# Performance work log

Measured on AMD Instinct MI355X. Metric: run time of the kernel, lower is better.

The kernel has to match this reference:

```python
import jax, jax.numpy as jnp
import numpy as np
from jax import lax

EPS = 1e-5

# Straight-through identity binarization (torch code mutates .data, so autograd
# sees binarized values but grads flow as identity to the latent weights/inputs).
def ste_sign(x):
    return x + lax.stop_gradient(jnp.sign(x) - x)

# SignActivation: sign forward, hard-tanh-style gradient (zero where |i| > 1).
@jax.custom_vjp
def sign_act(x):
    return jnp.sign(x)

def _sa_fwd(x):
    return jnp.sign(x), x

def _sa_bwd(x, g):
    return (jnp.where(jnp.abs(x) <= 1.0, g, 0.0),)

sign_act.defvjp(_sa_fwd, _sa_bwd)

def bn2d(x, gamma, beta):
    # training-mode BatchNorm2d: batch stats over (N,H,W), biased variance
    mean = jnp.mean(x, axis=(0, 2, 3), keepdims=True)
    var = jnp.var(x, axis=(0, 2, 3), keepdims=True)
    xn = (x - mean) * lax.rsqrt(var + EPS)
    return xn * gamma.reshape(1, -1, 1, 1) + beta.reshape(1, -1, 1, 1)

def bn1d(x, gamma, beta):
    mean = jnp.mean(x, axis=0, keepdims=True)
    var = jnp.var(x, axis=0, keepdims=True)
    xn = (x - mean) * lax.rsqrt(var + EPS)
    return xn * gamma[None, :] + beta[None, :]

def conv2d(x, w, stride, pad):
    return lax.conv_general_dilated(
        x, w, window_strides=(stride, stride),
        padding=((pad, pad), (pad, pad)),
        dimension_numbers=("NCHW", "OIHW", "NCHW"))


def setup_inputs() -> dict:
    key = jax.random.key(0)
    ks = jax.random.split(key, 4)
    width = 0.01
    x = jax.random.normal(ks[0], (8192, 1, 28, 28), dtype=jnp.float32)
    w1 = jax.random.normal(ks[1], (32, 1, 5, 5), dtype=jnp.float32) * width
    w2 = jax.random.normal(ks[2], (64, 32, 4, 4), dtype=jnp.float32) * width
    w3 = jax.random.normal(ks[3], (10, 64 * 64), dtype=jnp.float32) * width
    g1 = jnp.ones((32,), jnp.float32); b1 = jnp.zeros((32,), jnp.float32)
    g2 = jnp.ones((64,), jnp.float32); b2 = jnp.zeros((64,), jnp.float32)
    g3 = jnp.ones((10,), jnp.float32); b3 = jnp.zeros((10,), jnp.float32)
    return {"x": x, "w1": w1, "g1": g1, "b1": b1,
            "w2": w2, "g2": g2, "b2": b2,
            "w3": w3, "g3": g3, "b3": b3}


def reference(x, w1, g1, b1, w2, g2, b2, w3, g3, b3):
    # cv1: input channels = 1 != 3 -> input binarized; weight binarized
    h = conv2d(ste_sign(x), ste_sign(w1), stride=2, pad=2)   # [B,32,14,14]
    h = bn2d(h, g1, b1)
    h = sign_act(h)
    # cv2: input channels 32 != 3 -> binarized (no-op on +-1 values)
    h = conv2d(ste_sign(h), ste_sign(w2), stride=2, pad=2)   # [B,64,8,8]
    h = bn2d(h, g2, b2)
    h = sign_act(h)
    h = h.reshape(h.shape[0], -1)                            # [B,4096]
    # fc3: features 4096 != 784 -> binarized (no-op on +-1 values)
    h = jnp.dot(ste_sign(h), ste_sign(w3).T)                 # [B,10]
    h = bn1d(h, g3, b3)
    return h
```

## Files before the change

kernel.cpp:

```cpp
#include <hip/hip_runtime.h>
#include <stdint.h>


#define NB 8192
typedef unsigned long long ull;

#define OFF_C1  ((size_t)0)
#define SZ_C1   ((size_t)NB*6272)
#define OFF_C2  (OFF_C1 + SZ_C1)
#define SZ_C2   ((size_t)NB*4096)
#define OFF_FC  (OFF_C2 + SZ_C2)
#define SZ_FC   ((size_t)NB*10*4)
#define OFF_S1  (OFF_FC + SZ_FC)
#define OFF_S2  (OFF_S1 + 2048)
#define OFF_S3  (OFF_S2 + 8192)
#define OFF_W2B (OFF_S3 + 2048)
#define OFF_W3B (OFF_W2B + 4096)

__device__ inline void mk_thresh(double s, double t, int &T, int &flip) {
    if (s > 0.0) {
        int v = (int)floor(-t / s) - 2;
        for (int c = 0; c < 6; ++c) { if (s * (double)v + t > 0.0) break; ++v; }
        T = v; flip = 0;
    } else if (s < 0.0) {
        int v = (int)floor(-t / s) - 2;
        for (int c = 0; c < 6; ++c) { if (!(s * (double)v + t > 0.0)) break; ++v; }
        T = v; flip = 1;
    } else { T = -200; flip = (t > 0.0) ? 0 : 1; }
}
__device__ inline int clampT(int T, int lim) {
    return (T < -lim) ? -lim : (T > lim) ? lim : T;
}

__global__ __launch_bounds__(256) void kA_conv1(
    const float* __restrict__ x, const float* __restrict__ w1,
    const float* __restrict__ w2, const float* __restrict__ w3,
    int8_t* __restrict__ c1out, int* __restrict__ stats1,
    ull* __restrict__ w2bT, ull* __restrict__ w3b)
{
    const int tid = threadIdx.x, lane = tid & 63, wv = tid >> 6;

    if (blockIdx.x == 2048) {
        for (int m = wv; m < 10; m += 4) {
            const float* wp = w3 + (size_t)m*4096;
            ull mine = 0ull;
            for (int ch = 0; ch < 64; ++ch) {
                const ull bal = __ballot(wp[(size_t)ch*64 + lane] > 0.f);
                if (lane == ch) mine = bal;
            }
            w3b[m*64 + lane] = mine;
        }
        for (int t = tid; t < 512; t += 256) {
            const int idx = t >> 6, k = t & 63;
            const int u = idx >> 1, pr = idx & 1;
            uint32_t lo = 0u, hi = 0u;
            for (int c = 0; c < 32; ++c) {
                const float* wp = w2 + (((k*32 + c)*4 + u)*4 + 2*pr);
                lo |= (wp[0] > 0.f ? 1u : 0u) << c;
                hi |= (wp[1] > 0.f ? 1u : 0u) << c;
            }
            w2bT[t] = (ull)lo | ((ull)hi << 32);
        }
        return;
    }

    __shared__ ull sxb[4][16];
    __shared__ uint32_t wfilt[32];
    __shared__ uint32_t outb[4][1568];
    __shared__ int lsum[32], lsq[32];

    if (tid < 32) {
        uint32_t f = 0u;
        #pragma unroll
        for (int q = 0; q < 25; ++q) f |= (w1[tid*25 + q] > 0.f ? 1u : 0u) << q;
        wfilt[tid] = f;
        lsum[tid] = 0; lsq[tid] = 0;
    }
    __syncthreads();
    const int n = blockIdx.x*4 + wv;
    #pragma unroll
    for (int t = 0; t < 13; ++t) {
        const int idx = t*64 + lane;
        const float v = (idx < 784) ? x[(size_t)n*784 + idx] : -1.f;
        const ull bal = __ballot(v > 0.f);
        if (lane == t) sxb[wv][t] = bal;
    }
    if (lane == 13) sxb[wv][13] = 0ull;
    for (int t = 0; t < 4; ++t) {
        const int p = t*64 + lane;
        if (p < 196) {
            const int i = p / 14, j = p - i*14;
            const uint32_t cmask = (j == 0) ? 0x1Cu : (j == 13) ? 0x0Fu : 0x1Fu;
            uint32_t win = 0u, vm = 0u;
            #pragma unroll
            for (int u = 0; u < 5; ++u) {
                const int r = 2*i + u - 2;
                if (r >= 0 && r < 28) {
                    const int bp = 28*r, w0 = bp >> 6, sh = bp & 63;
                    const ull a = sxb[wv][w0], b = sxb[wv][w0+1];
                    uint32_t row = (uint32_t)((a >> sh) | ((b << 1) << (63 - sh)));
                    row = (row & 0x0FFFFFFFu) << 2;
                    win |= ((row >> (2*j)) & 31u) << (5*u);
                    vm  |= cmask << (5*u);
                }
            }
            const int nv = __popc(vm);
            uint32_t dw[8];
            #pragma unroll
            for (int d = 0; d < 8; ++d) dw[d] = 0u;
            #pragma unroll
            for (int c = 0; c < 32; ++c) {
                const int diff = __popc((win ^ wfilt[c]) & vm);
                const int o = nv - 2*diff;
                dw[c >> 2] |= (uint32_t)(o & 255) << (8*(c & 3));
            }
            #pragma unroll
            for (int d = 0; d < 8; ++d) outb[wv][p*8 + d] = dw[d];
        }
    }
    {
        int4* dst = (int4*)(c1out + (size_t)n*6272);
        const int4* src = (const int4*)&outb[wv][0];
        #pragma unroll
        for (int t = 0; t < 7; ++t) {
            const int idx = t*64 + lane;
            if (idx < 392) dst[idx] = src[idx];
        }
    }
    {
        const int ch = lane & 31, half = lane >> 5;
        const int8_t* ob = (const int8_t*)&outb[wv][0];
        int s = 0, q = 0;
        for (int p = half*98; p < half*98 + 98; ++p) {
            const int v = ob[p*32 + ch];
            s += v; q += v*v;
        }
        s += __shfl_xor(s, 32);
        q += __shfl_xor(q, 32);
        if (lane < 32) { atomicAdd(&lsum[lane], s); atomicAdd(&lsq[lane], q); }
    }
    __syncthreads();
    if (tid < 32) {
        const int shard = blockIdx.x & 7;
        atomicAdd(&stats1[(shard*32 + tid)*2 + 0], lsum[tid]);
        atomicAdd(&stats1[(shard*32 + tid)*2 + 1], lsq[tid]);
    }
}

__global__ __launch_bounds__(256) void kB_conv2(
    const int8_t* __restrict__ c1out, const int* __restrict__ stats1,
    const float* __restrict__ gm1, const float* __restrict__ bt1,
    const ull* __restrict__ w2bT,
    int8_t* __restrict__ c2out, ull* __restrict__ stats2)
{
    __shared__ ull BwU[4][14][8];
    __shared__ int sT1[4][32];
    __shared__ uint32_t cw[4][64][17];
    __shared__ int ssum[64], ssq[64];
    const int tid = threadIdx.x, lane = tid & 63, wv = tid >> 6;
    const int n = blockIdx.x*4 + wv;

    ull W[8];
    #pragma unroll
    for (int idx = 0; idx < 8; ++idx) W[idx] = w2bT[idx*64 + lane];

    if (tid < 64) { ssum[tid] = 0; ssq[tid] = 0; }
    int fl = 0;
    if (lane < 32) {
        long long s = 0, q = 0;
        for (int sh = 0; sh < 8; ++sh) {
            s += stats1[(sh*32 + lane)*2 + 0];
            q += stats1[(sh*32 + lane)*2 + 1];
        }
        const double N = 8192.0 * 196.0;
        const double mean = (double)s / N;
        const double var  = (double)q / N - mean*mean;
        const double a = (double)gm1[lane] / sqrt(var + 1e-5);
        const double b = (double)bt1[lane] - mean*a;
        int T; mk_thresh(a, b, T, fl);
        sT1[wv][lane] = clampT(T, 26);
    }
    const uint32_t flipn1 = ~(uint32_t)__ballot(fl != 0);
    __syncthreads();

    for (int t = lane; t < 196; t += 64) {
        const int r = t / 14, c = t - r*14;
        const uint4* src = (const uint4*)(c1out + ((size_t)n*196 + t)*32);
        const uint4 lo4 = src[0], hi4 = src[1];
        const uint32_t wsrc[8] = {lo4.x, lo4.y, lo4.z, lo4.w, hi4.x, hi4.y, hi4.z, hi4.w};
        uint32_t neg = 0u;
        #pragma unroll
        for (int d = 0; d < 8; ++d) {
            #pragma unroll
            for (int qq = 0; qq < 4; ++qq) {
                const int ch = d*4 + qq;
                const int v = (int)((int8_t)(wsrc[d] >> (8*qq)));
                neg |= ((uint32_t)(v - sT1[wv][ch]) >> 31) << ch;
            }
        }
        ((uint32_t*)&BwU[wv][r][0])[c] = neg ^ flipn1;
    }
    int s = 0, q = 0;
    #pragma unroll
    for (int i = 0; i < 8; ++i) {
        uint32_t packA = 0u;
        #pragma unroll
        for (int j = 0; j < 8; ++j) {
            int D = 0, nw = 0;
            #pragma unroll
            for (int u = 0; u < 4; ++u) {
                const int r = 2*i + u - 2;
                if (r < 0 || r > 13) continue;
                const ull* row = &BwU[wv][r][0];
                if (j >= 1) { D += __popcll(row[j-1] ^ W[2*u+0]); ++nw; }
                if (j <= 6) { D += __popcll(row[j]   ^ W[2*u+1]); ++nw; }
            }
            const int o = 32*nw - D;
            s += o; q += o*o;
            packA |= (uint32_t)(o & 255) << (8*(j & 3));
            if ((j & 3) == 3) { cw[wv][lane][2*i + (j >> 2)] = packA; packA = 0u; }
        }
    }
    atomicAdd(&ssum[lane], s);
    atomicAdd(&ssq[lane], q);
    {
        uint32_t* dst = (uint32_t*)(c2out + (size_t)n*4096);
        #pragma unroll
        for (int t = 0; t < 16; ++t) {
            const int g = t*64 + lane;
            dst[g] = cw[wv][g >> 4][g & 15];
        }
    }
    __syncthreads();
    if (tid < 64) {
        const int shard = blockIdx.x & 7;
        atomicAdd(&stats2[(shard*64 + tid)*2 + 0], (ull)(long long)ssum[tid]);
        atomicAdd(&stats2[(shard*64 + tid)*2 + 1], (ull)(long long)ssq[tid]);
    }
}

__global__ __launch_bounds__(256) void kC_fc(
    const int8_t* __restrict__ c2o, const float* __restrict__ gm2,
    const float* __restrict__ bt2, const ull* __restrict__ stats2,
    const ull* __restrict__ w3b,
    int* __restrict__ fc, ull* __restrict__ stats3)
{
    __shared__ int fco[4][10];
    __shared__ int s3[10], q3[10];
    const int tid = threadIdx.x, lane = tid & 63, wv = tid >> 6;
    if (tid < 10) { s3[tid] = 0; q3[tid] = 0; }
    int T2, fl;
    {
        long long ss = 0, qq = 0;
        for (int sh = 0; sh < 8; ++sh) {
            ss += (long long)stats2[(sh*64 + lane)*2 + 0];
            qq += (long long)stats2[(sh*64 + lane)*2 + 1];
        }
        const double N = 8192.0 * 64.0;
        const double mh = (double)ss / N;
        const double vh = (double)qq / N - mh*mh;
        const double a = (double)gm2[lane] / sqrt(4.0*vh + 1e-5);
        const double b = (double)bt2[lane] - 2.0*mh*a;
        int T; mk_thresh(2.0*a, b, T, fl);
        T2 = clampT(T, 200);
    }
    const ull flipn2 = ~__ballot(fl != 0);
    const int n = blockIdx.x*4 + wv;
    const uint4* src = (const uint4*)(c2o + (size_t)n*4096 + lane*64);
    uint32_t neglo = 0u, neghi = 0u;
    #pragma unroll
    for (int r4 = 0; r4 < 4; ++r4) {
        const uint4 v4 = src[r4];
        const uint32_t wsrc[4] = {v4.x, v4.y, v4.z, v4.w};
        #pragma unroll
        for (int c = 0; c < 4; ++c) {
            #pragma unroll
            for (int b = 0; b < 4; ++b) {
                const int p = r4*16 + c*4 + b;
                const int v = (int)((int8_t)(wsrc[c] >> (8*b)));
                const uint32_t bit = (uint32_t)(v - T2) >> 31;
                if (p < 32) neglo |= bit << p; else neghi |= bit << (p - 32);
            }
        }
    }
    const ull myw = ((ull)neglo | ((ull)neghi << 32)) ^ flipn2;
    uint32_t pk[5];
    #pragma unroll
    for (int t = 0; t < 5; ++t) {
        const uint32_t pa = (uint32_t)__popcll(myw ^ w3b[(2*t+0)*64 + lane]);
        const uint32_t pb = (uint32_t)__popcll(myw ^ w3b[(2*t+1)*64 + lane]);
        pk[t] = pa | (pb << 16);
    }
    #pragma unroll
    for (int off = 32; off >= 1; off >>= 1) {
        #pragma unroll
        for (int t = 0; t < 5; ++t) pk[t] += __shfl_xor(pk[t], off);
    }
    if (lane == 0) {
        #pragma unroll
        for (int m = 0; m < 10; ++m) {
            const int tot = (pk[m >> 1] >> (16*(m & 1))) & 0xFFFF;
            fco[wv][m] = 4096 - 2*tot;
        }
    }
    __syncthreads();
    if (tid < 40) {
        const int li = tid / 10, m = tid - li*10;
        const int o = fco[li][m];
        fc[(size_t)(blockIdx.x*4 + li)*10 + m] = o;
        atomicAdd(&s3[m], o);
        atomicAdd(&q3[m], o*o);
    }
    __syncthreads();
    if (tid < 10) {
        const int shard = blockIdx.x & 7;
        atomicAdd(&stats3[(shard*10 + tid)*2 + 0], (ull)(long long)s3[tid]);
        atomicAdd(&stats3[(shard*10 + tid)*2 + 1], (ull)(long long)q3[tid]);
    }
}

__global__ __launch_bounds__(256) void kD_apply(
    const int* __restrict__ fc, const float* __restrict__ gm3,
    const float* __restrict__ bt3, const ull* __restrict__ stats3,
    float* __restrict__ out)
{
    __shared__ float a3[10], b3[10];
    const int tid = threadIdx.x;
    if (tid < 10) {
        long long s = 0, q = 0;
        for (int sh = 0; sh < 8; ++sh) {
            s += (long long)stats3[(sh*10 + tid)*2 + 0];
            q += (long long)stats3[(sh*10 + tid)*2 + 1];
        }
        const double N = 8192.0;
        const double mean = (double)s / N;
        const double var  = (double)q / N - mean*mean;
        const double a = (double)gm3[tid] / sqrt(var + 1e-5);
        a3[tid] = (float)a;
        b3[tid] = (float)((double)bt3[tid] - mean*a);
    }
    __syncthreads();
    const int e = blockIdx.x*256 + tid;
    if (e < NB*10) {
        const int m = e % 10;
        out[e] = fmaf(a3[m], (float)fc[e], b3[m]);
    }
}

extern "C" void kernel_launch(void* const* d_in, const int* in_sizes, int n_in,
                              void* d_out, int out_size, void* d_ws, size_t ws_size,
                              hipStream_t stream)
{
    const float* x   = (const float*)d_in[0];
    const float* w1  = (const float*)d_in[1];
    const float* gm1 = (const float*)d_in[2];
    const float* bt1 = (const float*)d_in[3];
    const float* w2  = (const float*)d_in[4];
    const float* gm2 = (const float*)d_in[5];
    const float* bt2 = (const float*)d_in[6];
    const float* w3  = (const float*)d_in[7];
    const float* gm3 = (const float*)d_in[8];
    const float* bt3 = (const float*)d_in[9];
    char* ws = (char*)d_ws;
    int8_t* c1o = (int8_t*)(ws + OFF_C1);
    int8_t* c2o = (int8_t*)(ws + OFF_C2);
    int*    fcb = (int*)(ws + OFF_FC);
    int*    s1  = (int*)(ws + OFF_S1);
    ull*    s2  = (ull*)(ws + OFF_S2);
    ull*    s3  = (ull*)(ws + OFF_S3);
    ull*    w2bp = (ull*)(ws + OFF_W2B);
    ull*    w3bp = (ull*)(ws + OFF_W3B);

    hipMemsetAsync(ws + OFF_S1, 0, 12288, stream);
    kA_conv1<<<2049, 256, 0, stream>>>(x, w1, w2, w3, c1o, s1, w2bp, w3bp);
    kB_conv2<<<2048, 256, 0, stream>>>(c1o, s1, gm1, bt1, w2bp, c2o, s2);
    kC_fc   <<<2048, 256, 0, stream>>>(c2o, gm2, bt2, s2, w3bp, fcb, s3);
    kD_apply<<<320,  256, 0, stream>>>(fcb, gm3, bt3, s3, (float*)d_out);
}
```

Baseline: 181.6 us.

## Store binarized conv1 windows instead of int8 conv1 outputs; recompute in conv2

Conv1 now writes only the 25-bit input window per output position (1 KB per sample) rather than 32 int8 channel outputs (6.3 KB per sample). It computes the BN1 statistics directly in registers using readlane broadcasts instead of going through shared memory. Conv2 reloads the windows, recomputes the popcount conv1 outputs and thresholds them with ballots per position, which removes the large intermediate round trip through global memory. In exchange both kernels do redundant popcount work, and conv2 adds a 196-step serial loop per wave. Shared-memory staging and block-level syncs are also replaced by per-wave direct stores and atomics.

New measurement: 416.3 us. +129.2%, slower.

```diff
diff --git a/kernel.cpp b/kernel.cpp
--- a/kernel.cpp
+++ b/kernel.cpp
@@ -5,9 +5,9 @@
 #define NB 8192
 typedef unsigned long long ull;
 
-#define OFF_C1  ((size_t)0)
-#define SZ_C1   ((size_t)NB*6272)
-#define OFF_C2  (OFF_C1 + SZ_C1)
+#define OFF_WIN ((size_t)0)
+#define SZ_WIN  ((size_t)NB*1024)
+#define OFF_C2  (OFF_WIN + SZ_WIN)
 #define SZ_C2   ((size_t)NB*4096)
 #define OFF_FC  (OFF_C2 + SZ_C2)
 #define SZ_FC   ((size_t)NB*10*4)
@@ -32,10 +32,22 @@
     return (T < -lim) ? -lim : (T > lim) ? lim : T;
 }
 
+__device__ __forceinline__ void pos_consts(int p, uint32_t &vm, int &nv) {
+    const int i = p / 14, j = p - 14*i;
+    const uint32_t cmask = (j == 0) ? 0x1Cu : (j == 13) ? 0x0Fu : 0x1Fu;
+    vm = 0u;
+    #pragma unroll
+    for (int u = 0; u < 5; ++u) {
+        const int r = 2*i + u - 2;
+        if (r >= 0 && r < 28) vm |= cmask << (5*u);
+    }
+    nv = __popc(vm);
+}
+
 __global__ __launch_bounds__(256) void kA_conv1(
     const float* __restrict__ x, const float* __restrict__ w1,
     const float* __restrict__ w2, const float* __restrict__ w3,
-    int8_t* __restrict__ c1out, int* __restrict__ stats1,
+    uint32_t* __restrict__ wing, int* __restrict__ stats1,
     ull* __restrict__ w2bT, ull* __restrict__ w3b)
 {
     const int tid = threadIdx.x, lane = tid & 63, wv = tid >> 6;
@@ -65,98 +77,70 @@
     }
 
     __shared__ ull sxb[4][16];
-    __shared__ uint32_t wfilt[32];
-    __shared__ uint32_t outb[4][1568];
-    __shared__ int lsum[32], lsq[32];
-
-    if (tid < 32) {
-        uint32_t f = 0u;
-        #pragma unroll
-        for (int q = 0; q < 25; ++q) f |= (w1[tid*25 + q] > 0.f ? 1u : 0u) << q;
-        wfilt[tid] = f;
-        lsum[tid] = 0; lsq[tid] = 0;
-    }
-    __syncthreads();
     const int n = blockIdx.x*4 + wv;
+
+    uint32_t wf = 0u;
+    {
+        const int c = lane & 31;
+        #pragma unroll
+        for (int q = 0; q < 25; ++q) wf |= (w1[c*25 + q] > 0.f ? 1u : 0u) << q;
+    }
+    uint32_t blo = 0u, bhi = 0u;
     #pragma unroll
     for (int t = 0; t < 13; ++t) {
         const int idx = t*64 + lane;
         const float v = (idx < 784) ? x[(size_t)n*784 + idx] : -1.f;
         const ull bal = __ballot(v > 0.f);
-        if (lane == t) sxb[wv][t] = bal;
-    }
-    if (lane == 13) sxb[wv][13] = 0ull;
+        blo = (lane == t) ? (uint32_t)bal : blo;
+        bhi = (lane == t) ? (uint32_t)(bal >> 32) : bhi;
+    }
+    if (lane < 14) sxb[wv][lane] = (lane < 13) ? (((ull)bhi << 32) | blo) : 0ull;
+    uint32_t win_t[4];
+    #pragma unroll
     for (int t = 0; t < 4; ++t) {
         const int p = t*64 + lane;
+        uint32_t win = 0u;
         if (p < 196) {
             const int i = p / 14, j = p - i*14;
-            const uint32_t cmask = (j == 0) ? 0x1Cu : (j == 13) ? 0x0Fu : 0x1Fu;
-            uint32_t win = 0u, vm = 0u;
             #pragma unroll
             for (int u = 0; u < 5; ++u) {
                 const int r = 2*i + u - 2;
-                if (r >= 0 && r < 28) {
-                    const int bp = 28*r, w0 = bp >> 6, sh = bp & 63;
-                    const ull a = sxb[wv][w0], b = sxb[wv][w0+1];
-                    uint32_t row = (uint32_t)((a >> sh) | ((b << 1) << (63 - sh)));
-                    row = (row & 0x0FFFFFFFu) << 2;
-                    win |= ((row >> (2*j)) & 31u) << (5*u);
-                    vm  |= cmask << (5*u);
-                }
-            }
-            const int nv = __popc(vm);
-            uint32_t dw[8];
-            #pragma unroll
-            for (int d = 0; d < 8; ++d) dw[d] = 0u;
-            #pragma unroll
-            for (int c = 0; c < 32; ++c) {
-                const int diff = __popc((win ^ wfilt[c]) & vm);
-                const int o = nv - 2*diff;
-                dw[c >> 2] |= (uint32_t)(o & 255) << (8*(c & 3));
-            }
-            #pragma unroll
-            for (int d = 0; d < 8; ++d) outb[wv][p*8 + d] = dw[d];
-        }
-    }
-    {
-        int4* dst = (int4*)(c1out + (size_t)n*6272);
-        const int4* src = (const int4*)&outb[wv][0];
-        #pragma unroll
-        for (int t = 0; t < 7; ++t) {
-            const int idx = t*64 + lane;
-            if (idx < 392) dst[idx] = src[idx];
-        }
-    }
-    {
-        const int ch = lane & 31, half = lane >> 5;
-        const int8_t* ob = (const int8_t*)&outb[wv][0];
-        int s = 0, q = 0;
-        for (int p = half*98; p < half*98 + 98; ++p) {
-            const int v = ob[p*32 + ch];
-            s += v; q += v*v;
-        }
-        s += __shfl_xor(s, 32);
-        q += __shfl_xor(q, 32);
-        if (lane < 32) { atomicAdd(&lsum[lane], s); atomicAdd(&lsq[lane], q); }
-    }
-    __syncthreads();
-    if (tid < 32) {
-        const int shard = blockIdx.x & 7;
-        atomicAdd(&stats1[(shard*32 + tid)*2 + 0], lsum[tid]);
-        atomicAdd(&stats1[(shard*32 + tid)*2 + 1], lsq[tid]);
+                const int rc = (r < 0) ? 0 : (r > 27) ? 27 : r;
+                const int bp = 28*rc, w0 = bp >> 6, sh = bp & 63;
+                const ull a = sxb[wv][w0], b = sxb[wv][w0+1];
+                uint32_t row = (uint32_t)((a >> sh) | ((b << 1) << (63 - sh)));
+                row = (row & 0x0FFFFFFFu) << 2;
+                const uint32_t bits = ((row >> (2*j)) & 31u) << (5*u);
+                win |= (r >= 0 && r < 28) ? bits : 0u;
+            }
+            wing[(size_t)n*256 + p] = win;
+        }
+        win_t[t] = win;
+    }
+    int s = 0, q = 0;
+    #pragma unroll
+    for (int p = 0; p < 196; ++p) {
+        const uint32_t WW = (uint32_t)__builtin_amdgcn_readlane((int)win_t[p >> 6], p & 63);
+        uint32_t vm; int nv; pos_consts(p, vm, nv);
+        const int d = __popc((WW ^ wf) & vm);
+        const int o = nv - 2*d;
+        s += o; q += o*o;
+    }
+    if (lane < 32) {
+        const int shard = (blockIdx.x*4 + wv) & 7;
+        atomicAdd(&stats1[(shard*32 + lane)*2 + 0], s);
+        atomicAdd(&stats1[(shard*32 + lane)*2 + 1], q);
     }
 }
 
 __global__ __launch_bounds__(256) void kB_conv2(
-    const int8_t* __restrict__ c1out, const int* __restrict__ stats1,
+    const uint32_t* __restrict__ wing, const float* __restrict__ w1,
+    const int* __restrict__ stats1,
     const float* __restrict__ gm1, const float* __restrict__ bt1,
     const ull* __restrict__ w2bT,
     int8_t* __restrict__ c2out, ull* __restrict__ stats2)
 {
-    __shared__ ull BwU[4][14][8];
-    __shared__ int sT1[4][32];
-    __shared__ uint32_t cw[4][64][17];
-    __shared__ int ssum[64], ssq[64];
+    __shared__ uint32_t Bw[4][256];
     const int tid = threadIdx.x, lane = tid & 63, wv = tid >> 6;
     const int n = blockIdx.x*4 + wv;
 
@@ -164,43 +148,58 @@
     #pragma unroll
     for (int idx = 0; idx < 8; ++idx) W[idx] = w2bT[idx*64 + lane];
 
-    if (tid < 64) { ssum[tid] = 0; ssq[tid] = 0; }
-    int fl = 0;
-    if (lane < 32) {
-        long long s = 0, q = 0;
+    const int c = lane & 31;
+    uint32_t wf = 0u;
+    #pragma unroll
+    for (int qq = 0; qq < 25; ++qq) wf |= (w1[c*25 + qq] > 0.f ? 1u : 0u) << qq;
+    int T1, fl;
+    {
+        long long ss = 0, qs = 0;
         for (int sh = 0; sh < 8; ++sh) {
-            s += stats1[(sh*32 + lane)*2 + 0];
-            q += stats1[(sh*32 + lane)*2 + 1];
+            ss += stats1[(sh*32 + c)*2 + 0];
+            qs += stats1[(sh*32 + c)*2 + 1];
         }
         const double N = 8192.0 * 196.0;
-        const double mean = (double)s / N;
-        const double var  = (double)q / N - mean*mean;
-        const double a = (double)gm1[lane] / sqrt(var + 1e-5);
-        const double b = (double)bt1[lane] - mean*a;
+        const double mean = (double)ss / N;
+        const double var  = (double)qs / N - mean*mean;
+        const double a = (double)gm1[c] / sqrt(var + 1e-5);
+        const double b = (double)bt1[c] - mean*a;
         int T; mk_thresh(a, b, T, fl);
-        sT1[wv][lane] = clampT(T, 26);
-    }
-    const uint32_t flipn1 = ~(uint32_t)__ballot(fl != 0);
-    __syncthreads();
-
-    for (int t = lane; t < 196; t += 64) {
-        const int r = t / 14, c = t - r*14;
-        const uint4* src = (const uint4*)(c1out + ((size_t)n*196 + t)*32);
-        const uint4 lo4 = src[0], hi4 = src[1];
-        const uint32_t wsrc[8] = {lo4.x, lo4.y, lo4.z, lo4.w, hi4.x, hi4.y, hi4.z, hi4.w};
-        uint32_t neg = 0u;
-        #pragma unroll
-        for (int d = 0; d < 8; ++d) {
-            #pragma unroll
-            for (int qq = 0; qq < 4; ++qq) {
-                const int ch = d*4 + qq;
-                const int v = (int)((int8_t)(wsrc[d] >> (8*qq)));
-                neg |= ((uint32_t)(v - sT1[wv][ch]) >> 31) << ch;
-            }
-        }
-        ((uint32_t*)&BwU[wv][r][0])[c] = neg ^ flipn1;
-    }
+        T1 = clampT(T, 26);
+    }
+    const uint32_t flipw = (uint32_t)__ballot(fl != 0);
+    const int thr9  = (9  - T1) >> 1, thr12 = (12 - T1) >> 1;
+    const int thr15 = (15 - T1) >> 1, thr16 = (16 - T1) >> 1;
+    const int thr20 = (20 - T1) >> 1, thr25 = (25 - T1) >> 1;
+
+    uint32_t wint[4];
+    #pragma unroll
+    for (int t = 0; t < 4; ++t) wint[t] = wing[(size_t)n*256 + t*64 + lane];
+
+    uint32_t bw0 = 0u, bw1 = 0u, bw2 = 0u, bw3 = 0u;
+    #pragma unroll
+    for (int p = 0; p < 196; ++p) {
+        const uint32_t WW = (uint32_t)__builtin_amdgcn_readlane((int)wint[p >> 6], p & 63);
+        uint32_t vm; int nv; pos_consts(p, vm, nv);
+        const int d = __popc((WW ^ wf) & vm);
+        const int thr = (nv == 9) ? thr9 : (nv == 12) ? thr12 : (nv == 15) ? thr15
+                      : (nv == 16) ? thr16 : (nv == 20) ? thr20 : thr25;
+        const uint32_t word = (uint32_t)__ballot(d <= thr) ^ flipw;
+        const int t = p >> 6, l = p & 63;
+        const bool sel = (lane == l);
+        if (t == 0)      bw0 = sel ? word : bw0;
+        else if (t == 1) bw1 = sel ? word : bw1;
+        else if (t == 2) bw2 = sel ? word : bw2;
+        else             bw3 = sel ? word : bw3;
+    }
+    Bw[wv][0*64 + lane] = bw0;
+    Bw[wv][1*64 + lane] = bw1;
+    Bw[wv][2*64 + lane] = bw2;
+    Bw[wv][3*64 + lane] = bw3;
+    __builtin_amdgcn_s_waitcnt(0);
+
     int s = 0, q = 0;
+    uint32_t od[16];
     #pragma unroll
     for (int i = 0; i < 8; ++i) {
         uint32_t packA = 0u;
@@ -211,31 +210,24 @@
             for (int u = 0; u < 4; ++u) {
                 const int r = 2*i + u - 2;
                 if (r < 0 || r > 13) continue;
-                const ull* row = &BwU[wv][r][0];
-                if (j >= 1) { D += __popcll(row[j-1] ^ W[2*u+0]); ++nw; }
-                if (j <= 6) { D += __popcll(row[j]   ^ W[2*u+1]); ++nw; }
+                if (j >= 1) { D += __popcll(*(const ull*)&Bw[wv][r*14 + 2*j - 2] ^ W[2*u+0]); ++nw; }
+                if (j <= 6) { D += __popcll(*(const ull*)&Bw[wv][r*14 + 2*j]     ^ W[2*u+1]); ++nw; }
             }
             const int o = 32*nw - D;
             s += o; q += o*o;
             packA |= (uint32_t)(o & 255) << (8*(j & 3));
-            if ((j & 3) == 3) { cw[wv][lane][2*i + (j >> 2)] = packA; packA = 0u; }
-        }
-    }
-    atomicAdd(&ssum[lane], s);
-    atomicAdd(&ssq[lane], q);
-    {
-        uint32_t* dst = (uint32_t*)(c2out + (size_t)n*4096);
-        #pragma unroll
-        for (int t = 0; t < 16; ++t) {
-            const int g = t*64 + lane;
-            dst[g] = cw[wv][g >> 4][g & 15];
-        }
-    }
-    __syncthreads();
-    if (tid < 64) {
-        const int shard = blockIdx.x & 7;
-        atomicAdd(&stats2[(shard*64 + tid)*2 + 0], (ull)(long long)ssum[tid]);
-        atomicAdd(&stats2[(shard*64 + tid)*2 + 1], (ull)(long long)ssq[tid]);
+            if ((j & 3) == 3) { od[2*i + (j >> 2)] = packA; packA = 0u; }
+        }
+    }
+    {
+        uint32_t* dst = (uint32_t*)(c2out + (size_t)n*4096) + lane*16;
+        #pragma unroll
+        for (int t = 0; t < 16; ++t) dst[t] = od[t];
+    }
+    {
+        const int shard = (blockIdx.x*4 + wv) & 7;
+        atomicAdd(&stats2[(shard*64 + lane)*2 + 0], (ull)(long long)s);
+        atomicAdd(&stats2[(shard*64 + lane)*2 + 1], (ull)(long long)q);
     }
 }
 
@@ -273,11 +265,11 @@
         const uint4 v4 = src[r4];
         const uint32_t wsrc[4] = {v4.x, v4.y, v4.z, v4.w};
         #pragma unroll
-        for (int c = 0; c < 4; ++c) {
+        for (int cc = 0; cc < 4; ++cc) {
             #pragma unroll
             for (int b = 0; b < 4; ++b) {
-                const int p = r4*16 + c*4 + b;
-                const int v = (int)((int8_t)(wsrc[c] >> (8*b)));
+                const int p = r4*16 + cc*4 + b;
+                const int v = (int)((int8_t)(wsrc[cc] >> (8*b)));
                 const uint32_t bit = (uint32_t)(v - T2) >> 31;
                 if (p < 32) neglo |= bit << p; else neghi |= bit << (p - 32);
             }
@@ -362,7 +354,7 @@
     const float* gm3 = (const float*)d_in[8];
     const float* bt3 = (const float*)d_in[9];
     char* ws = (char*)d_ws;
-    int8_t* c1o = (int8_t*)(ws + OFF_C1);
+    uint32_t* wing = (uint32_t*)(ws + OFF_WIN);
     int8_t* c2o = (int8_t*)(ws + OFF_C2);
     int*    fcb = (int*)(ws + OFF_FC);
     int*    s1  = (int*)(ws + OFF_S1);
@@ -371,9 +363,9 @@
     ull*    w2bp = (ull*)(ws + OFF_W2B);
     ull*    w3bp = (ull*)(ws + OFF_W3B);
 
-    hipMemsetAsync(ws + OFF_S1, 0, 12288, stream);
-    kA_conv1<<<2049, 256, 0, stream>>>(x, w1, w2, w3, c1o, s1, w2bp, w3bp);
-    kB_conv2<<<2048, 256, 0, stream>>>(c1o, s1, gm1, bt1, w2bp, c2o, s2);
+    (void)hipMemsetAsync(ws + OFF_S1, 0, 12288, stream);
+    kA_conv1<<<2049, 256, 0, stream>>>(x, w1, w2, w3, wing, s1, w2bp, w3bp);
+    kB_conv2<<<2048, 256, 0, stream>>>(wing, w1, s1, gm1, bt1, w2bp, c2o, s2);
     kC_fc   <<<2048, 256, 0, stream>>>(c2o, gm2, bt2, s2, w3bp, fcb, s3);
     kD_apply<<<320,  256, 0, stream>>>(fcb, gm3, bt3, s3, (float*)d_out);
 }
```

## Write conv outputs directly to global, register-stage conv2 rows, vectorize stats

Applied to the files above, without the earlier changes.

In conv1, each position's 32 channel bytes are stored to global memory as soon as they are computed, replacing the later LDS-to-global copy. The per-channel stat reduction now reads whole dwords and reduces them with shuffles. In conv2, the staging through the shared cw array is removed: thresholds are kept in registers and passed by shuffle, input row pairs are loaded from LDS into double-buffered register arrays, and outputs go straight to global as 8-byte stores. Launch bounds are tightened to 4 blocks. This cuts LDS traffic and barriers but raises register pressure, and the global stores are narrower and more scattered.

Measured after the change: 189.0 us. 1.04x slower.

```diff
diff --git a/kernel.cpp b/kernel.cpp
--- a/kernel.cpp
+++ b/kernel.cpp
@@ -116,28 +116,41 @@
             }
             #pragma unroll
             for (int d = 0; d < 8; ++d) outb[wv][p*8 + d] = dw[d];
+            uint4* dst = (uint4*)(c1out + (size_t)n*6272 + (size_t)p*32);
+            dst[0] = make_uint4(dw[0], dw[1], dw[2], dw[3]);
+            dst[1] = make_uint4(dw[4], dw[5], dw[6], dw[7]);
         }
     }
     {
-        int4* dst = (int4*)(c1out + (size_t)n*6272);
-        const int4* src = (const int4*)&outb[wv][0];
-        #pragma unroll
-        for (int t = 0; t < 7; ++t) {
+        int s4[4] = {0,0,0,0}, q4[4] = {0,0,0,0};
+        const uint32_t* ob32 = &outb[wv][0];
+        #pragma unroll
+        for (int t = 0; t < 25; ++t) {
             const int idx = t*64 + lane;
-            if (idx < 392) dst[idx] = src[idx];
-        }
-    }
-    {
-        const int ch = lane & 31, half = lane >> 5;
-        const int8_t* ob = (const int8_t*)&outb[wv][0];
-        int s = 0, q = 0;
-        for (int p = half*98; p < half*98 + 98; ++p) {
-            const int v = ob[p*32 + ch];
-            s += v; q += v*v;
-        }
-        s += __shfl_xor(s, 32);
-        q += __shfl_xor(q, 32);
-        if (lane < 32) { atomicAdd(&lsum[lane], s); atomicAdd(&lsq[lane], q); }
+            if (idx < 1568) {
+                const uint32_t dwv = ob32[idx];
+                #pragma unroll
+                for (int qq = 0; qq < 4; ++qq) {
+                    const int v = (int)((int8_t)(dwv >> (8*qq)));
+                    s4[qq] += v; q4[qq] += v*v;
+                }
+            }
+        }
+        #pragma unroll
+        for (int off = 8; off <= 32; off <<= 1) {
+            #pragma unroll
+            for (int qq = 0; qq < 4; ++qq) {
+                s4[qq] += __shfl_xor(s4[qq], off);
+                q4[qq] += __shfl_xor(q4[qq], off);
+            }
+        }
+        if (lane < 8) {
+            #pragma unroll
+            for (int qq = 0; qq < 4; ++qq) {
+                atomicAdd(&lsum[lane*4 + qq], s4[qq]);
+                atomicAdd(&lsq[lane*4 + qq], q4[qq]);
+            }
+        }
     }
     __syncthreads();
     if (tid < 32) {
@@ -147,44 +160,54 @@
     }
 }
 
-__global__ __launch_bounds__(256) void kB_conv2(
+__global__ __launch_bounds__(256, 4) void kB_conv2(
     const int8_t* __restrict__ c1out, const int* __restrict__ stats1,
     const float* __restrict__ gm1, const float* __restrict__ bt1,
     const ull* __restrict__ w2bT,
     int8_t* __restrict__ c2out, ull* __restrict__ stats2)
 {
-    __shared__ ull BwU[4][14][8];
-    __shared__ int sT1[4][32];
-    __shared__ uint32_t cw[4][64][17];
+    __shared__ uint32_t Bw[4][14][16];
     __shared__ int ssum[64], ssq[64];
     const int tid = threadIdx.x, lane = tid & 63, wv = tid >> 6;
     const int n = blockIdx.x*4 + wv;
 
-    ull W[8];
-    #pragma unroll
-    for (int idx = 0; idx < 8; ++idx) W[idx] = w2bT[idx*64 + lane];
-
+    uint32_t Wlo[8], Whi[8];
+    #pragma unroll
+    for (int idx = 0; idx < 8; ++idx) {
+        const uint2 w = ((const uint2*)w2bT)[idx*64 + lane];
+        Wlo[idx] = w.x; Whi[idx] = w.y;
+    }
     if (tid < 64) { ssum[tid] = 0; ssq[tid] = 0; }
-    int fl = 0;
-    if (lane < 32) {
-        long long s = 0, q = 0;
+
+    const int c = lane & 31;
+    int T1, fl;
+    {
+        long long ss = 0, qs = 0;
         for (int sh = 0; sh < 8; ++sh) {
-            s += stats1[(sh*32 + lane)*2 + 0];
-            q += stats1[(sh*32 + lane)*2 + 1];
+            ss += stats1[(sh*32 + c)*2 + 0];
+            qs += stats1[(sh*32 + c)*2 + 1];
         }
         const double N = 8192.0 * 196.0;
-        const double mean = (double)s / N;
-        const double var  = (double)q / N - mean*mean;
-        const double a = (double)gm1[lane] / sqrt(var + 1e-5);
-        const double b = (double)bt1[lane] - mean*a;
+        const double mean = (double)ss / N;
+        const double var  = (double)qs / N - mean*mean;
+        const double a = (double)gm1[c] / sqrt(var + 1e-5);
+        const double b = (double)bt1[c] - mean*a;
         int T; mk_thresh(a, b, T, fl);
-        sT1[wv][lane] = clampT(T, 26);
-    }
-    const uint32_t flipn1 = ~(uint32_t)__ballot(fl != 0);
+        T1 = clampT(T, 26);
+    }
+    const uint32_t flipn1 = ~(uint32_t)__ballot((lane < 32) && (fl != 0));
+    uint32_t tp[8];
+    {
+        uint32_t myb = ((uint32_t)(T1 & 255)) << (8*(lane & 3));
+        myb |= __shfl_xor(myb, 1);
+        myb |= __shfl_xor(myb, 2);
+        #pragma unroll
+        for (int k = 0; k < 8; ++k) tp[k] = __shfl(myb, 4*k);
+    }
     __syncthreads();
 
     for (int t = lane; t < 196; t += 64) {
-        const int r = t / 14, c = t - r*14;
+        const int r = t / 14, cc = t - r*14;
         const uint4* src = (const uint4*)(c1out + ((size_t)n*196 + t)*32);
         const uint4 lo4 = src[0], hi4 = src[1];
         const uint32_t wsrc[8] = {lo4.x, lo4.y, lo4.z, lo4.w, hi4.x, hi4.y, hi4.z, hi4.w};
@@ -195,42 +218,61 @@
             for (int qq = 0; qq < 4; ++qq) {
                 const int ch = d*4 + qq;
                 const int v = (int)((int8_t)(wsrc[d] >> (8*qq)));
-                neg |= ((uint32_t)(v - sT1[wv][ch]) >> 31) << ch;
-            }
-        }
-        ((uint32_t*)&BwU[wv][r][0])[c] = neg ^ flipn1;
+                const int T = (int)((int8_t)(tp[d] >> (8*qq)));
+                neg |= ((uint32_t)(v - T) >> 31) << ch;
+            }
+        }
+        Bw[wv][r][cc] = neg ^ flipn1;
+    }
+    __builtin_amdgcn_s_waitcnt(0);
+
+    uint32_t bufA[28], bufB[28];
+#define LOADPAIR(BUF, K)                                            \
+    {                                                               \
+        _Pragma("unroll")                                           \
+        for (int t2 = 0; t2 < 14; ++t2) {                           \
+            BUF[t2]      = Bw[wv][2*(K)][t2];                       \
+            BUF[14 + t2] = Bw[wv][2*(K)+1][t2];                     \
+        }                                                           \
+    }
+#define UTERM(BUF, BASE, UU)                                                          \
+    {                                                                                 \
+        if (j >= 1) { D += __popc(BUF[(BASE)+2*j-2] ^ Wlo[2*(UU)])                    \
+                         + __popc(BUF[(BASE)+2*j-1] ^ Whi[2*(UU)]);   ++nw; }         \
+        if (j <= 6) { D += __popc(BUF[(BASE)+2*j]   ^ Wlo[2*(UU)+1])                  \
+                         + __popc(BUF[(BASE)+2*j+1] ^ Whi[2*(UU)+1]); ++nw; }         \
     }
     int s = 0, q = 0;
+    int8_t* outbase = c2out + (size_t)n*4096 + lane*64;
     #pragma unroll
     for (int i = 0; i < 8; ++i) {
-        uint32_t packA = 0u;
+        if (i == 0) { LOADPAIR(bufA, 0) }
+        else if (i < 7) {
+            if (i & 1) { LOADPAIR(bufB, i) } else { LOADPAIR(bufA, i) }
+        }
+        uint32_t o0 = 0u, o1 = 0u;
         #pragma unroll
         for (int j = 0; j < 8; ++j) {
             int D = 0, nw = 0;
-            #pragma unroll
-            for (int u = 0; u < 4; ++u) {
-                const int r = 2*i + u - 2;
-                if (r < 0 || r > 13) continue;
-                const ull* row = &BwU[wv][r][0];
-                if (j >= 1) { D += __popcll(row[j-1] ^ W[2*u+0]); ++nw; }
-                if (j <= 6) { D += __popcll(row[j]   ^ W[2*u+1]); ++nw; }
+            if (i >= 1) {
+                if ((i-1) & 1) { UTERM(bufB, 0, 0) UTERM(bufB, 14, 1) }
+                else           { UTERM(bufA, 0, 0) UTERM(bufA, 14, 1) }
+            }
+            if (i <= 6) {
+                if (i & 1) { UTERM(bufB, 0, 2) UTERM(bufB, 14, 3) }
+                else       { UTERM(bufA, 0, 2) UTERM(bufA, 14, 3) }
             }
             const int o = 32*nw - D;
             s += o; q += o*o;
-            packA |= (uint32_t)(o & 255) << (8*(j & 3));
-            if ((j & 3) == 3) { cw[wv][lane][2*i + (j >> 2)] = packA; packA = 0u; }
-        }
-    }
+            if (j < 4) o0 |= (uint32_t)(o & 255) << (8*j);
+            else       o1 |= (uint32_t)(o & 255) << (8*(j-4));
+        }
+        *(uint2*)(outbase + i*8) = make_uint2(o0, o1);
+    }
+#undef LOADPAIR
+#undef UTERM
     atomicAdd(&ssum[lane], s);
     atomicAdd(&ssq[lane], q);
-    {
-        uint32_t* dst = (uint32_t*)(c2out + (size_t)n*4096);
-        #pragma unroll
-        for (int t = 0; t < 16; ++t) {
-            const int g = t*64 + lane;
-            dst[g] = cw[wv][g >> 4][g & 15];
-        }
-    }
     __syncthreads();
     if (tid < 64) {
         const int shard = blockIdx.x & 7;
@@ -273,11 +315,11 @@
         const uint4 v4 = src[r4];
         const uint32_t wsrc[4] = {v4.x, v4.y, v4.z, v4.w};
         #pragma unroll
-        for (int c = 0; c < 4; ++c) {
+        for (int cc = 0; cc < 4; ++cc) {
             #pragma unroll
             for (int b = 0; b < 4; ++b) {
-                const int p = r4*16 + c*4 + b;
-                const int v = (int)((int8_t)(wsrc[c] >> (8*b)));
+                const int p = r4*16 + cc*4 + b;
+                const int v = (int)((int8_t)(wsrc[cc] >> (8*b)));
                 const uint32_t bit = (uint32_t)(v - T2) >> 31;
                 if (p < 32) neglo |= bit << p; else neghi |= bit << (p - 32);
             }
@@ -371,7 +413,7 @@
     ull*    w2bp = (ull*)(ws + OFF_W2B);
     ull*    w3bp = (ull*)(ws + OFF_W3B);
 
-    hipMemsetAsync(ws + OFF_S1, 0, 12288, stream);
+    (void)hipMemsetAsync(ws + OFF_S1, 0, 12288, stream);
     kA_conv1<<<2049, 256, 0, stream>>>(x, w1, w2, w3, c1o, s1, w2bp, w3bp);
     kB_conv2<<<2048, 256, 0, stream>>>(c1o, s1, gm1, bt1, w2bp, c2o, s2);
     kC_fc   <<<2048, 256, 0, stream>>>(c2o, gm2, bt2, s2, w3bp, fcb, s3);
```
